# Performance work log

Hardware: AMD Instinct MI355X
Metric: run time of the kernel (lower is better)

The kernel has to match this reference:

```python
import jax, jax.numpy as jnp
import numpy as np

K = 3          # kernel_size
PAD = 1        # padding for offset conv and deform conv
UPS = 2        # ConvTranspose2d stride
EPS = 1e-5     # BatchNorm eps


def _conv2d(x, w, b, pad):
    y = jax.lax.conv_general_dilated(x, w, (1, 1), [(pad, pad), (pad, pad)],
                                     dimension_numbers=('NCHW', 'OIHW', 'NCHW'))
    return y + b[None, :, None, None]


def _deform_conv(x, offsets, w, b):
    # torchvision DeformConv2d semantics, stride=1, pad=1, dilation=1
    B, C, H, W = x.shape
    KK = K * K
    off = offsets.reshape(B, KK, 2, H, W)  # [:, kk, 0]=dy, [:, kk, 1]=dx
    ki, kj = jnp.meshgrid(jnp.arange(K), jnp.arange(K), indexing='ij')
    py = (jnp.arange(H) - PAD)[None, None, :, None] + ki.ravel()[None, :, None, None] + off[:, :, 0]
    px = (jnp.arange(W) - PAD)[None, None, None, :] + kj.ravel()[None, :, None, None] + off[:, :, 1]
    y0f = jnp.floor(py); x0f = jnp.floor(px)
    ly = py - y0f; lx = px - x0f
    y0 = y0f.astype(jnp.int32); x0 = x0f.astype(jnp.int32)
    xf = x.reshape(B, C, H * W)

    def corner(yy, xx, wgt):
        valid = (yy >= 0) & (yy < H) & (xx >= 0) & (xx < W)
        idx = jnp.clip(yy, 0, H - 1) * W + jnp.clip(xx, 0, W - 1)      # [B,KK,H,W]
        v = jax.vmap(lambda f, i: f[:, i])(xf, idx)                     # [B,C,KK,H,W]
        return v * (wgt * valid)[:, None]

    s = (corner(y0, x0, (1 - ly) * (1 - lx)) + corner(y0, x0 + 1, (1 - ly) * lx)
         + corner(y0 + 1, x0, ly * (1 - lx)) + corner(y0 + 1, x0 + 1, ly * lx))
    out = jnp.einsum('bckhw,ock->bohw', s, w.reshape(w.shape[0], C, KK))
    return out + b[None, :, None, None]


def _conv_transpose(x, w, b):
    # torch ConvTranspose2d(stride=UPS, padding=0); torch weight is [C_in, C_out, K, K]
    wf = jnp.flip(jnp.transpose(w, (1, 0, 2, 3)), (2, 3))
    y = jax.lax.conv_general_dilated(x, wf, (1, 1), [(K - 1, K - 1)] * 2,
                                     lhs_dilation=(UPS, UPS),
                                     dimension_numbers=('NCHW', 'OIHW', 'NCHW'))
    return y + b[None, :, None, None]


def setup_inputs() -> dict:
    key = jax.random.key(0)
    ks = jax.random.split(key, 8)
    B, Cin, Cout, H, W = 16, 64, 128, 64, 64
    s = 0.05
    return {
        'x': jax.random.normal(ks[0], (B, Cin, H, W), jnp.float32),
        'w_off': jax.random.normal(ks[1], (2 * K * K, Cin, K, K), jnp.float32) * s,
        'b_off': jax.random.normal(ks[2], (2 * K * K,), jnp.float32) * s,
        'w_def': jax.random.normal(ks[3], (Cout, Cin, K, K), jnp.float32) * s,
        'b_def': jax.random.normal(ks[4], (Cout,), jnp.float32) * s,
        'w_up': jax.random.normal(ks[5], (Cout, Cout, K, K), jnp.float32) * s,
        'b_up': jax.random.normal(ks[6], (Cout,), jnp.float32) * s,
        'gamma': jnp.ones((Cout,), jnp.float32),
        'beta': jnp.zeros((Cout,), jnp.float32),
    }


def reference(x, w_off, b_off, w_def, b_def, w_up, b_up, gamma, beta):
    offsets = _conv2d(x, w_off, b_off, PAD)
    feats = _deform_conv(x, offsets, w_def, b_def)
    y = _conv_transpose(feats, w_up, b_up)
    # BatchNorm2d (training mode, biased batch stats) + ReLU
    mu = jnp.mean(y, axis=(0, 2, 3), keepdims=True)
    var = jnp.var(y, axis=(0, 2, 3), keepdims=True)
    yn = (y - mu) * jax.lax.rsqrt(var + EPS)
    yn = yn * gamma[None, :, None, None] + beta[None, :, None, None]
    return jax.nn.relu(yn)
```

## Files before the change

kernel.cpp:

```cpp
#include <hip/hip_runtime.h>
#include <math.h>

#define PADC 1
#define CIN  64
#define COUT 128
#define IH   64
#define IW   64
#define NB   16
#define OYX  129
#define OXP  136
#define NOFF 18
#define SPO  (OYX * OYX)
#define BNEPS 1e-5f
#define NBLK_CT (NB * 65)

typedef __attribute__((ext_vector_type(8))) short bf16x8;
typedef __attribute__((ext_vector_type(4))) float f32x4;

static __device__ __forceinline__ unsigned short f2bf(float f) {
    unsigned int b = __float_as_uint(f);
    unsigned int r = (b + 0x7FFFu + ((b >> 16) & 1u)) >> 16;
    return (unsigned short)r;
}
static __device__ __forceinline__ float bf2f(unsigned short u) {
    return __uint_as_float((unsigned int)u << 16);
}

__global__ __launch_bounds__(256) void k_pre(
    const float* __restrict__ x, const float* __restrict__ w_def,
    const float* __restrict__ w_up, const float* __restrict__ w_off,
    unsigned short* __restrict__ xt, unsigned short* __restrict__ WDF,
    unsigned short* __restrict__ WB, unsigned short* __restrict__ WOF)
{
    __shared__ unsigned short t[64][66];
    const int tid = threadIdx.x;
    if (blockIdx.x < 1024) {
        const int h = blockIdx.x & 63, b = blockIdx.x >> 6;
        const int w = tid & 63, cq = tid >> 6;
        #pragma unroll
        for (int p = 0; p < 16; ++p) {
            const int c = p * 4 + cq;
            t[w][c] = f2bf(x[((size_t)((b * 64 + c) * 64) + h) * 64 + w]);
        }
        __syncthreads();
        const int w2 = tid >> 2, q = tid & 3;
        unsigned int pk[8];
        #pragma unroll
        for (int m = 0; m < 8; ++m)
            pk[m] = (unsigned int)t[w2][q * 16 + 2 * m] | ((unsigned int)t[w2][q * 16 + 2 * m + 1] << 16);
        uint4* dst = (uint4*)(xt + ((size_t)((b * 64 + h) * 64) + w2) * 64 + q * 16);
        dst[0] = uint4{pk[0], pk[1], pk[2], pk[3]};
        dst[1] = uint4{pk[4], pk[5], pk[6], pk[7]};
        return;
    }
    int idx = (blockIdx.x - 1024) * 256 + tid;
    if (idx < 73728) {
        const int j = idx & 7;
        const int n = (idx >> 3) & 127;
        const int g = idx >> 10;
        const int kg = g & 3, ks = (g >> 2) & 1, kk = g >> 3;
        const int c = ks * 32 + kg * 8 + j;
        WDF[idx] = f2bf(w_def[(n * CIN + c) * 9 + kk]);
    }
    const int i2 = idx - 73728;
    if (i2 >= 0 && i2 < 147456) {
        const int j = i2 & 7;
        const int n = (i2 >> 3) & 127;
        int ky, kx, ci;
        if (i2 < 65536) {
            const int k = (i2 >> 10) * 8 + j;
            ky = (k >> 8) ? 0 : 2;
            kx = ((k >> 7) & 1) ? 0 : 2;
            ci = k & 127;
        } else if (i2 < 98304) {
            const int k = ((i2 - 65536) >> 10) * 8 + j;
            ky = 1;
            kx = (k >> 7) ? 0 : 2;
            ci = k & 127;
        } else if (i2 < 131072) {
            const int k = ((i2 - 98304) >> 10) * 8 + j;
            ky = (k >> 7) ? 0 : 2;
            kx = 1;
            ci = k & 127;
        } else {
            const int k = ((i2 - 131072) >> 10) * 8 + j;
            ky = 1; kx = 1;
            ci = k & 127;
        }
        WB[i2] = f2bf(w_up[((ci * COUT + n) * 3 + ky) * 3 + kx]);
    }
    const int i3 = idx - 221184;
    if (i3 >= 0 && i3 < 18432) {
        const int j = i3 & 7;
        const int n = (i3 >> 3) & 31;
        const int g = i3 >> 8;
        const int kg = g & 3, s = g >> 2;
        const int c  = (s & 1) * 32 + kg * 8 + j;
        const int kk = s >> 1;
        const int ki = kk / 3, kj = kk - 3 * ki;
        WOF[i3] = (n < NOFF) ? f2bf(w_off[((n * CIN + c) * 3 + ki) * 3 + kj]) : (unsigned short)0;
    }
}

__global__ __launch_bounds__(64, 4) void k_offset_mfma(
    const unsigned short* __restrict__ xt, const unsigned short* __restrict__ WOF,
    const float* __restrict__ b_off, float* __restrict__ offs2)
{
    const int l  = threadIdx.x;
    const int ml = l & 15;
    const int kg = l >> 4;
    const int r  = blockIdx.x & 7;
    const int i  = blockIdx.x >> 3;
    const int b  = 2 * r + (i >> 8);
    const int hq = i & 255;
    const int q  = hq & 3;
    const int h  = hq >> 2;
    const int w  = q * 16 + ml;
    const unsigned short* xb = xt + (size_t)b * (IH * IW * CIN);

    const f32x4 fz = {0.f, 0.f, 0.f, 0.f};
    f32x4 acc0 = fz, acc1 = fz;

    #pragma unroll
    for (int s = 0; s < 18; ++s) {
        const int kk = s >> 1;
        const int ki = kk / 3, kj = kk - 3 * ki;
        const int c0 = (s & 1) * 32 + kg * 8;
        const int yy = h - PADC + ki;
        const int xx = w - PADC + kj;
        const bf16x8 b0 = *(const bf16x8*)(WOF + (size_t)(((s * 4 + kg) * 32 + ml) * 8));
        const bf16x8 b1 = *(const bf16x8*)(WOF + (size_t)(((s * 4 + kg) * 32 + 16 + ml) * 8));
        bf16x8 a = {0, 0, 0, 0, 0, 0, 0, 0};
        if (yy >= 0 && yy < IH && xx >= 0 && xx < IW)
            a = *(const bf16x8*)(xb + (size_t)((yy * IW + xx) * CIN) + c0);
        acc0 = __builtin_amdgcn_mfma_f32_16x16x32_bf16(a, b0, acc0, 0, 0, 0);
        acc1 = __builtin_amdgcn_mfma_f32_16x16x32_bf16(a, b1, acc1, 0, 0, 0);
    }
    #pragma unroll
    for (int nt = 0; nt < 2; ++nt) {
        const int oc = nt * 16 + ml;
        if (oc < NOFF) {
            const float bias = b_off[oc];
            const f32x4 av = nt ? acc1 : acc0;
            #pragma unroll
            for (int j = 0; j < 4; ++j) {
                const int wd = q * 16 + kg * 4 + j;
                offs2[((size_t)((b * IH + h) * IW) + wd) * NOFF + oc] = av[j] + bias;
            }
        }
    }
}

__global__ __launch_bounds__(64, 4) void k_deform_mfma(
    const unsigned short* __restrict__ xt, const float* __restrict__ offs2,
    const unsigned short* __restrict__ WDF, const float* __restrict__ b_def,
    unsigned short* __restrict__ feats_bf)
{
    const int l  = threadIdx.x;
    const int ml = l & 15;
    const int kg = l >> 4;
    const int r  = blockIdx.x & 7;
    const int i  = blockIdx.x >> 3;
    const int b  = 2 * r + (i >> 8);
    const int hq = i & 255;
    const int q  = hq & 3;
    const int h  = hq >> 2;
    const int w  = q * 16 + ml;

    const unsigned short* xb = xt + (size_t)b * (IH * IW * CIN);

    float2 dd[9];
    {
        const float* op = offs2 + ((size_t)((b * IH + h) * IW) + w) * NOFF;
        #pragma unroll
        for (int kk = 0; kk < 9; ++kk)
            dd[kk] = *(const float2*)(op + 2 * kk);
    }

    const f32x4 fz = {0.f, 0.f, 0.f, 0.f};
    f32x4 acc[8];
    #pragma unroll
    for (int nt = 0; nt < 8; ++nt) acc[nt] = fz;

    #pragma unroll
    for (int kk = 0; kk < 9; ++kk) {
        const int ki = kk / 3, kj = kk - 3 * ki;
        const float py = (float)(h - PADC + ki) + dd[kk].x;
        const float px = (float)(w - PADC + kj) + dd[kk].y;
        const float y0f = floorf(py), x0f = floorf(px);
        const float ly = py - y0f, lx = px - x0f;
        const int y0 = (int)y0f, x0 = (int)x0f;
        const float wy[2] = {1.f - ly, ly};
        const float wx[2] = {1.f - lx, lx};
        int   cidx[4];
        float cwgt[4];
        #pragma unroll
        for (int cy = 0; cy < 2; ++cy)
            #pragma unroll
            for (int cx = 0; cx < 2; ++cx) {
                const int yy = y0 + cy, xx = x0 + cx;
                const bool v = (yy >= 0) & (yy < IH) & (xx >= 0) & (xx < IW);
                cidx[cy * 2 + cx] = v ? ((yy * IW + xx) * CIN) : 0;
                cwgt[cy * 2 + cx] = v ? (wy[cy] * wx[cx]) : 0.f;
            }
        #pragma unroll
        for (int ks = 0; ks < 2; ++ks) {
            const int c0 = ks * 32 + kg * 8;
            uint4 cv[4];
            #pragma unroll
            for (int cp = 0; cp < 4; ++cp)
                cv[cp] = *(const uint4*)(xb + cidx[cp] + c0);
            float sf[8] = {0.f, 0.f, 0.f, 0.f, 0.f, 0.f, 0.f, 0.f};
            #pragma unroll
            for (int cp = 0; cp < 4; ++cp) {
                const float wg = cwgt[cp];
                const unsigned int u0 = cv[cp].x, u1 = cv[cp].y, u2 = cv[cp].z, u3 = cv[cp].w;
                sf[0] += wg * __uint_as_float(u0 << 16);
                sf[1] += wg * __uint_as_float(u0 & 0xFFFF0000u);
                sf[2] += wg * __uint_as_float(u1 << 16);
                sf[3] += wg * __uint_as_float(u1 & 0xFFFF0000u);
                sf[4] += wg * __uint_as_float(u2 << 16);
                sf[5] += wg * __uint_as_float(u2 & 0xFFFF0000u);
                sf[6] += wg * __uint_as_float(u3 << 16);
                sf[7] += wg * __uint_as_float(u3 & 0xFFFF0000u);
            }
            union { unsigned short us[8]; bf16x8 v; } pa;
            #pragma unroll
            for (int j = 0; j < 8; ++j) pa.us[j] = f2bf(sf[j]);
            #pragma unroll
            for (int half = 0; half < 2; ++half) {
                bf16x8 bfr[4];
                #pragma unroll
                for (int nn = 0; nn < 4; ++nn)
                    bfr[nn] = *(const bf16x8*)(WDF + ((size_t)((kk * 8 + ks * 4 + kg) * 128) + (half * 4 + nn) * 16 + ml) * 8);
                #pragma unroll
                for (int nn = 0; nn < 4; ++nn)
                    acc[half * 4 + nn] = __builtin_amdgcn_mfma_f32_16x16x32_bf16(pa.v, bfr[nn], acc[half * 4 + nn], 0, 0, 0);
            }
        }
    }
    #pragma unroll
    for (int nt = 0; nt < 8; ++nt) {
        const int o = nt * 16 + ml;
        const float bias = b_def[o];
        #pragma unroll
        for (int j = 0; j < 4; ++j) {
            const int wd = q * 16 + kg * 4 + j;
            feats_bf[((size_t)((b * IH + h) * IW) + wd) * COUT + o] = f2bf(acc[nt][j] + bias);
        }
    }
}

__global__ __launch_bounds__(256) void k_convT_mfma(
    const unsigned short* __restrict__ feats_bf, const unsigned short* __restrict__ WB,
    unsigned short* __restrict__ y_bf, float* __restrict__ partials)
{
    __shared__ __align__(16) char smem[33792];

    const int tid = threadIdx.x;
    const int l   = tid & 63;
    const int wv  = tid >> 6;
    const int ml  = l & 15;
    const int kg  = l >> 4;
    const int blk = blockIdx.x;
    const int r_  = blk & 7;
    const int i_  = blk >> 3;
    const int b   = 2 * r_ + (i_ >= 65 ? 1 : 0);
    const int t   = (i_ >= 65) ? (i_ - 65) : i_;

    for (int r = 0; r < 2; ++r) {
        char* dstbase = smem + r * 16896;
        const int iy = t - 1 + r;
        if (iy < 0 || iy > 63) {
            for (int i = tid; i < 1056; i += 256)
                *(uint4*)(dstbase + i * 16) = uint4{0, 0, 0, 0};
        } else {
            const unsigned short* src = feats_bf + (size_t)(b * IH + iy) * (IW * COUT);
            for (int i = tid; i < 1024; i += 256) {
                const uint4 v = *(const uint4*)(src + i * 8);
                const int G = 16 + i;
                const int phys = G ^ ((G >> 4) & 7);
                *(uint4*)(dstbase + phys * 16) = v;
            }
            if (tid < 32) {
                const int G = (tid < 16) ? tid : (1024 + tid);
                const int phys = G ^ ((G >> 4) & 7);
                *(uint4*)(dstbase + phys * 16) = uint4{0, 0, 0, 0};
            }
        }
    }
    __syncthreads();

    const int n0 = wv * 32;
    const f32x4 fz = {0.f, 0.f, 0.f, 0.f};
    float sacc[2] = {0.f, 0.f}, qacc[2] = {0.f, 0.f};

    #pragma unroll 1
    for (int p = 0; p < 2; ++p) {
        if (p == 1 && t == 64) break;
        const int oy = 2 * t + p;
        const unsigned short* segG0 = WB + (p ? 65536 : 0);
        const unsigned short* segG1 = WB + (p ? 131072 : 98304);
        const int nK0 = p ? 8 : 16;
        const int nK1 = p ? 4 : 8;

        f32x4 acc0[5][2], acc1[4][2];
        #pragma unroll
        for (int m = 0; m < 5; ++m) { acc0[m][0] = fz; acc0[m][1] = fz; }
        #pragma unroll
        for (int m = 0; m < 4; ++m) { acc1[m][0] = fz; acc1[m][1] = fz; }

        for (int ks = 0; ks < nK0; ++ks) {
            const int kk   = ks * 32 + kg * 8;
            const int slot = p ? 1 : (kk >> 8);
            const int kb   = (kk & 255) >> 3;
            const bf16x8 b0 = *(const bf16x8*)(segG0 + ((ks * 4 + kg) * 128 + n0 + ml) * 8);
            const bf16x8 b1 = *(const bf16x8*)(segG0 + ((ks * 4 + kg) * 128 + n0 + 16 + ml) * 8);
            #pragma unroll
            for (int mt = 0; mt < 5; ++mt) {
                int tx = mt * 16 + ml; if (tx > 64) tx = 64;
                const int G = tx * 16 + kb;
                const int phys = G ^ ((G >> 4) & 7);
                const bf16x8 a = *(const bf16x8*)(smem + slot * 16896 + phys * 16);
                acc0[mt][0] = __builtin_amdgcn_mfma_f32_16x16x32_bf16(a, b0, acc0[mt][0], 0, 0, 0);
                acc0[mt][1] = __builtin_amdgcn_mfma_f32_16x16x32_bf16(a, b1, acc0[mt][1], 0, 0, 0);
            }
        }
        for (int ks = 0; ks < nK1; ++ks) {
            const int kk   = ks * 32 + kg * 8;
            const int slot = p ? 1 : (kk >> 7);
            const int kb   = (kk & 127) >> 3;
            const bf16x8 b0 = *(const bf16x8*)(segG1 + ((ks * 4 + kg) * 128 + n0 + ml) * 8);
            const bf16x8 b1 = *(const bf16x8*)(segG1 + ((ks * 4 + kg) * 128 + n0 + 16 + ml) * 8);
            #pragma unroll
            for (int mt = 0; mt < 4; ++mt) {
                const int tx = mt * 16 + ml;
                const int G = 16 + tx * 16 + kb;
                const int phys = G ^ ((G >> 4) & 7);
                const bf16x8 a = *(const bf16x8*)(smem + slot * 16896 + phys * 16);
                acc1[mt][0] = __builtin_amdgcn_mfma_f32_16x16x32_bf16(a, b0, acc1[mt][0], 0, 0, 0);
                acc1[mt][1] = __builtin_amdgcn_mfma_f32_16x16x32_bf16(a, b1, acc1[mt][1], 0, 0, 0);
            }
        }

        #pragma unroll
        for (int nt = 0; nt < 2; ++nt) {
            const int co = n0 + nt * 16 + ml;
            unsigned int* drow32 = (unsigned int*)(y_bf + ((size_t)(b * COUT + co) * OYX + oy) * OXP);
            #pragma unroll
            for (int mt = 0; mt < 4; ++mt) {
                unsigned int pk[4];
                #pragma unroll
                for (int j = 0; j < 4; ++j) {
                    const float ve = acc0[mt][nt][j];
                    const float vo = acc1[mt][nt][j];
                    pk[j] = (unsigned int)f2bf(ve) | ((unsigned int)f2bf(vo) << 16);
                    sacc[nt] += ve + vo;
                    qacc[nt] += ve * ve + vo * vo;
                }
                *(uint4*)(drow32 + mt * 16 + kg * 4) = uint4{pk[0], pk[1], pk[2], pk[3]};
            }
            if (kg == 0) {
                const float ve = acc0[4][nt][0];
                drow32[64] = (unsigned int)f2bf(ve);
                sacc[nt] += ve;
                qacc[nt] += ve * ve;
            }
        }
    }

    #pragma unroll
    for (int nt = 0; nt < 2; ++nt) {
        float ss = sacc[nt], qq = qacc[nt];
        ss += __shfl_xor(ss, 16, 64); qq += __shfl_xor(qq, 16, 64);
        ss += __shfl_xor(ss, 32, 64); qq += __shfl_xor(qq, 32, 64);
        if (kg == 0) {
            float* pp = partials + ((size_t)blk * COUT + n0 + nt * 16 + ml) * 2;
            pp[0] = ss; pp[1] = qq;
        }
    }
}

__global__ __launch_bounds__(256) void k_bn_final(const float* __restrict__ partials,
                                                  float* __restrict__ stats)
{
    const int c = blockIdx.x;
    const int tid = threadIdx.x;
    float s = 0.f, q = 0.f;
    for (int i = tid; i < NBLK_CT; i += 256) {
        const float* pp = partials + ((size_t)i * COUT + c) * 2;
        s += pp[0]; q += pp[1];
    }
    __shared__ float rs[256], rq[256];
    rs[tid] = s; rq[tid] = q;
    __syncthreads();
    for (int off = 128; off > 0; off >>= 1) {
        if (tid < off) { rs[tid] += rs[tid + off]; rq[tid] += rq[tid + off]; }
        __syncthreads();
    }
    if (tid == 0) {
        const float n = (float)(NB * SPO);
        const float mean = rs[0] / n;
        const float var  = rq[0] / n - mean * mean;
        stats[c] = mean;
        stats[COUT + c] = rsqrtf(var + BNEPS);
    }
}

__global__ __launch_bounds__(256) void k_bn_apply(
    const unsigned short* __restrict__ y_bf, float* __restrict__ y,
    const float* __restrict__ stats,
    const float* __restrict__ gamma, const float* __restrict__ beta)
{
    const int v = blockIdx.x * 256 + threadIdx.x;
    const int rid = v / 17;
    const int c   = v - rid * 17;
    const int co  = (rid / OYX) & (COUT - 1);
    const float mean = stats[co], rstd = stats[COUT + co];
    const float ga = gamma[co], be = beta[co];
    const int ox0 = c * 8;

    const uint4 u = *(const uint4*)(y_bf + (size_t)rid * OXP + ox0);
    const unsigned int uu[4] = {u.x, u.y, u.z, u.w};
    float* dst = y + (size_t)rid * OYX + ox0;
    const int nv = (c < 16) ? 8 : 1;
    #pragma unroll
    for (int m = 0; m < 4; ++m) {
        float v0 = bf2f((unsigned short)(uu[m] & 0xFFFFu));
        float v1 = bf2f((unsigned short)(uu[m] >> 16));
        v0 = fmaxf((v0 - mean) * rstd * ga + be, 0.f);
        v1 = fmaxf((v1 - mean) * rstd * ga + be, 0.f);
        if (2 * m < nv)     dst[2 * m]     = v0;
        if (2 * m + 1 < nv) dst[2 * m + 1] = v1;
    }
}

extern "C" void kernel_launch(void* const* d_in, const int* in_sizes, int n_in,
                              void* d_out, int out_size, void* d_ws, size_t ws_size,
                              hipStream_t stream)
{
    const float* x     = (const float*)d_in[0];
    const float* w_off = (const float*)d_in[1];
    const float* b_off = (const float*)d_in[2];
    const float* w_def = (const float*)d_in[3];
    const float* b_def = (const float*)d_in[4];
    const float* w_up  = (const float*)d_in[5];
    const float* b_up  = (const float*)d_in[6];  (void)b_up;
    const float* gamma = (const float*)d_in[7];
    const float* beta  = (const float*)d_in[8];
    float* y = (float*)d_out;

    float* ws       = (float*)d_ws;
    float* stats    = ws;
    float* partials = stats + 256;
    float* offs2    = partials + 528384;
    unsigned short* xt       = (unsigned short*)(offs2 + 1179648);
    unsigned short* WDF      = xt + 4194304;
    unsigned short* feats_bf = WDF + 73728;
    unsigned short* WB       = feats_bf + 8388608;
    unsigned short* WOF      = WB + 147456;
    unsigned short* y_bf     = WOF + 18432;

    k_pre          <<<dim3(1960),   dim3(256), 0, stream>>>(x, w_def, w_up, w_off, xt, WDF, WB, WOF);
    k_offset_mfma  <<<dim3(4096),   dim3(64),  0, stream>>>(xt, WOF, b_off, offs2);
    k_deform_mfma  <<<dim3(4096),   dim3(64),  0, stream>>>(xt, offs2, WDF, b_def, feats_bf);
    k_convT_mfma   <<<dim3(NBLK_CT),dim3(256), 0, stream>>>(feats_bf, WB, y_bf, partials);
    k_bn_final     <<<dim3(128),    dim3(256), 0, stream>>>(partials, stats);
    k_bn_apply     <<<dim3(17544),  dim3(256), 0, stream>>>(y_bf, y, stats, gamma, beta);
}
```

Before: 161.4 us.

## Split deform conv channel reduction across two waves with LDS reduction

The deformable conv kernel now runs two wavefronts per block. Each wave handles half of the 64 input channels (split-K), where previously one wave looped over both halves. The partial MFMA accumulators are exchanged through shared memory, and each wave writes half of the output channels. This doubles wave-level parallelism and halves the per-wave serial gather and MFMA chain. In exchange it adds an LDS round trip, a block barrier, and duplicated offset and bilinear-weight computation in each wave.

Measured after the change: 173.2 us. +7.3%, slower.

```diff
diff --git a/kernel.cpp b/kernel.cpp
--- a/kernel.cpp
+++ b/kernel.cpp
@@ -151,14 +151,18 @@
     }
 }
 
-__global__ __launch_bounds__(64, 4) void k_deform_mfma(
+__global__ __launch_bounds__(128, 6) void k_deform_mfma(
     const unsigned short* __restrict__ xt, const float* __restrict__ offs2,
     const unsigned short* __restrict__ WDF, const float* __restrict__ b_def,
     unsigned short* __restrict__ feats_bf)
 {
-    const int l  = threadIdx.x;
-    const int ml = l & 15;
-    const int kg = l >> 4;
+    __shared__ f32x4 red[2][4][64];
+
+    const int tid = threadIdx.x;
+    const int ws  = tid >> 6;
+    const int l   = tid & 63;
+    const int ml  = l & 15;
+    const int kg  = l >> 4;
     const int r  = blockIdx.x & 7;
     const int i  = blockIdx.x >> 3;
     const int b  = 2 * r + (i >> 8);
@@ -168,6 +172,7 @@
     const int w  = q * 16 + ml;
 
     const unsigned short* xb = xt + (size_t)b * (IH * IW * CIN);
+    const int c0 = ws * 32 + kg * 8;
 
     float2 dd[9];
     {
@@ -203,50 +208,72 @@
                 cidx[cy * 2 + cx] = v ? ((yy * IW + xx) * CIN) : 0;
                 cwgt[cy * 2 + cx] = v ? (wy[cy] * wx[cx]) : 0.f;
             }
-        #pragma unroll
-        for (int ks = 0; ks < 2; ++ks) {
-            const int c0 = ks * 32 + kg * 8;
-            uint4 cv[4];
-            #pragma unroll
-            for (int cp = 0; cp < 4; ++cp)
-                cv[cp] = *(const uint4*)(xb + cidx[cp] + c0);
-            float sf[8] = {0.f, 0.f, 0.f, 0.f, 0.f, 0.f, 0.f, 0.f};
-            #pragma unroll
-            for (int cp = 0; cp < 4; ++cp) {
-                const float wg = cwgt[cp];
-                const unsigned int u0 = cv[cp].x, u1 = cv[cp].y, u2 = cv[cp].z, u3 = cv[cp].w;
-                sf[0] += wg * __uint_as_float(u0 << 16);
-                sf[1] += wg * __uint_as_float(u0 & 0xFFFF0000u);
-                sf[2] += wg * __uint_as_float(u1 << 16);
-                sf[3] += wg * __uint_as_float(u1 & 0xFFFF0000u);
-                sf[4] += wg * __uint_as_float(u2 << 16);
-                sf[5] += wg * __uint_as_float(u2 & 0xFFFF0000u);
-                sf[6] += wg * __uint_as_float(u3 << 16);
-                sf[7] += wg * __uint_as_float(u3 & 0xFFFF0000u);
-            }
-            union { unsigned short us[8]; bf16x8 v; } pa;
-            #pragma unroll
-            for (int j = 0; j < 8; ++j) pa.us[j] = f2bf(sf[j]);
-            #pragma unroll
-            for (int half = 0; half < 2; ++half) {
-                bf16x8 bfr[4];
-                #pragma unroll
-                for (int nn = 0; nn < 4; ++nn)
-                    bfr[nn] = *(const bf16x8*)(WDF + ((size_t)((kk * 8 + ks * 4 + kg) * 128) + (half * 4 + nn) * 16 + ml) * 8);
-                #pragma unroll
-                for (int nn = 0; nn < 4; ++nn)
-                    acc[half * 4 + nn] = __builtin_amdgcn_mfma_f32_16x16x32_bf16(pa.v, bfr[nn], acc[half * 4 + nn], 0, 0, 0);
-            }
-        }
-    }
-    #pragma unroll
-    for (int nt = 0; nt < 8; ++nt) {
-        const int o = nt * 16 + ml;
-        const float bias = b_def[o];
-        #pragma unroll
-        for (int j = 0; j < 4; ++j) {
-            const int wd = q * 16 + kg * 4 + j;
-            feats_bf[((size_t)((b * IH + h) * IW) + wd) * COUT + o] = f2bf(acc[nt][j] + bias);
+        uint4 cv[4];
+        #pragma unroll
+        for (int cp = 0; cp < 4; ++cp)
+            cv[cp] = *(const uint4*)(xb + cidx[cp] + c0);
+        float sf[8] = {0.f, 0.f, 0.f, 0.f, 0.f, 0.f, 0.f, 0.f};
+        #pragma unroll
+        for (int cp = 0; cp < 4; ++cp) {
+            const float wg = cwgt[cp];
+            const unsigned int u0 = cv[cp].x, u1 = cv[cp].y, u2 = cv[cp].z, u3 = cv[cp].w;
+            sf[0] += wg * __uint_as_float(u0 << 16);
+            sf[1] += wg * __uint_as_float(u0 & 0xFFFF0000u);
+            sf[2] += wg * __uint_as_float(u1 << 16);
+            sf[3] += wg * __uint_as_float(u1 & 0xFFFF0000u);
+            sf[4] += wg * __uint_as_float(u2 << 16);
+            sf[5] += wg * __uint_as_float(u2 & 0xFFFF0000u);
+            sf[6] += wg * __uint_as_float(u3 << 16);
+            sf[7] += wg * __uint_as_float(u3 & 0xFFFF0000u);
+        }
+        union { unsigned short us[8]; bf16x8 v; } pa;
+        #pragma unroll
+        for (int j = 0; j < 8; ++j) pa.us[j] = f2bf(sf[j]);
+        #pragma unroll
+        for (int half = 0; half < 2; ++half) {
+            bf16x8 bfr[4];
+            #pragma unroll
+            for (int nn = 0; nn < 4; ++nn)
+                bfr[nn] = *(const bf16x8*)(WDF + ((size_t)((kk * 8 + ws * 4 + kg) * 128) + (half * 4 + nn) * 16 + ml) * 8);
+            #pragma unroll
+            for (int nn = 0; nn < 4; ++nn)
+                acc[half * 4 + nn] = __builtin_amdgcn_mfma_f32_16x16x32_bf16(pa.v, bfr[nn], acc[half * 4 + nn], 0, 0, 0);
+        }
+    }
+
+    if (ws == 0) {
+        #pragma unroll
+        for (int nn = 0; nn < 4; ++nn) red[1][nn][l] = acc[4 + nn];
+    } else {
+        #pragma unroll
+        for (int nn = 0; nn < 4; ++nn) red[0][nn][l] = acc[nn];
+    }
+    __syncthreads();
+    if (ws == 0) {
+        #pragma unroll
+        for (int nn = 0; nn < 4; ++nn) {
+            const int o = nn * 16 + ml;
+            const f32x4 r2 = red[0][nn][l];
+            const float bias = b_def[o];
+            #pragma unroll
+            for (int j = 0; j < 4; ++j) {
+                const int wd = q * 16 + kg * 4 + j;
+                feats_bf[((size_t)((b * IH + h) * IW) + wd) * COUT + o] =
+                    f2bf(acc[nn][j] + r2[j] + bias);
+            }
+        }
+    } else {
+        #pragma unroll
+        for (int nn = 0; nn < 4; ++nn) {
+            const int o = (4 + nn) * 16 + ml;
+            const f32x4 r2 = red[1][nn][l];
+            const float bias = b_def[o];
+            #pragma unroll
+            for (int j = 0; j < 4; ++j) {
+                const int wd = q * 16 + kg * 4 + j;
+                feats_bf[((size_t)((b * IH + h) * IW) + wd) * COUT + o] =
+                    f2bf(acc[4 + nn][j] + r2[j] + bias);
+            }
         }
     }
 }
@@ -463,7 +490,7 @@
 
     k_pre          <<<dim3(1960),   dim3(256), 0, stream>>>(x, w_def, w_up, w_off, xt, WDF, WB, WOF);
     k_offset_mfma  <<<dim3(4096),   dim3(64),  0, stream>>>(xt, WOF, b_off, offs2);
-    k_deform_mfma  <<<dim3(4096),   dim3(64),  0, stream>>>(xt, offs2, WDF, b_def, feats_bf);
+    k_deform_mfma  <<<dim3(4096),   dim3(128), 0, stream>>>(xt, offs2, WDF, b_def, feats_bf);
     k_convT_mfma   <<<dim3(NBLK_CT),dim3(256), 0, stream>>>(feats_bf, WB, y_bf, partials);
     k_bn_final     <<<dim3(128),    dim3(256), 0, stream>>>(partials, stats);
     k_bn_apply     <<<dim3(17544),  dim3(256), 0, stream>>>(y_bf, y, stats, gamma, beta);
```
